# Kernel tuning notes

Measured on AMD Instinct MI355X. Metric: run time of the kernel, lower is better.

Reference implementation:

```python
import jax, jax.numpy as jnp
import numpy as np

B, S, D = 16, 2048, 128


def setup_inputs() -> dict:
    k = jax.random.key(0)
    k1, k2, k3, k4 = jax.random.split(k, 4)
    query = jax.random.normal(k1, (B, S, D), dtype=jnp.float32)
    key = jax.random.normal(k2, (B, S, D), dtype=jnp.float32)
    value = jax.random.normal(k3, (B, S, D), dtype=jnp.float32)
    # per-query tensor-valued inverse scale; shift away from zero for stable division
    inv_scale_factor = jax.random.uniform(k4, (B, S, 1), dtype=jnp.float32) + 0.5
    dropout_p = jnp.float32(0.1)
    return {"query": query, "key": key, "value": value,
            "inv_scale_factor": inv_scale_factor, "dropout_p": dropout_p}


def reference(query, key, value, inv_scale_factor, dropout_p):
    # QK^T: [B, Sq, Sk]
    qk = jnp.einsum('bqd,bkd->bqk', query, key)
    # tensor-valued scale divide (broadcast [B, Sq, 1] over keys)
    scaled_qk = qk / inv_scale_factor
    softmax_qk = jax.nn.softmax(scaled_qk, axis=-1)
    # dropout with a fixed RNG key (deterministic reference)
    keep_prob = 1.0 - dropout_p
    mask = jax.random.bernoulli(jax.random.key(42), keep_prob, softmax_qk.shape)
    dropout_qk = jnp.where(mask, softmax_qk / keep_prob, jnp.float32(0.0))
    # AV: [B, Sq, Dv]
    return jnp.einsum('bqk,bkv->bqv', dropout_qk, value)
```

## Files before the change

kernel.cpp:

```cpp
#include <hip/hip_runtime.h>
#include <stdint.h>


#define B_ 16
#define S_ 2048
#define D_ 128
#define TQ 128
#define TK 64
#define NT (S_ / TK)
#define KSTR 136
#define VSTR 72
#define PSTR 40

typedef float f32x4 __attribute__((ext_vector_type(4)));
typedef _Float16 f16x8 __attribute__((ext_vector_type(8)));
typedef _Float16 f16x2 __attribute__((ext_vector_type(2)));

union F32R { float4 q[4]; float f[16]; };

#define DPP_ROR(x, ctrl) \
  __int_as_float(__builtin_amdgcn_update_dpp(0, __float_as_int(x), (ctrl), 0xf, 0xf, true))
__device__ __forceinline__ float row16_max(float x) {
  x = fmaxf(x, DPP_ROR(x, 0x128));
  x = fmaxf(x, DPP_ROR(x, 0x124));
  x = fmaxf(x, DPP_ROR(x, 0x122));
  x = fmaxf(x, DPP_ROR(x, 0x121));
  return x;
}
__device__ __forceinline__ float row16_sum(float x) {
  x += DPP_ROR(x, 0x128);
  x += DPP_ROR(x, 0x124);
  x += DPP_ROR(x, 0x122);
  x += DPP_ROR(x, 0x121);
  return x;
}

__device__ __forceinline__ uint2 threefry2x32_0_42(uint32_t x0, uint32_t x1) {
  const uint32_t k0 = 0u, k1 = 42u;
  const uint32_t k2 = 0x1BD11BDAu ^ k0 ^ k1;
  x0 += k0; x1 += k1;
#define TFR(r) { x0 += x1; x1 = __builtin_rotateleft32(x1, r); x1 ^= x0; }
  TFR(13) TFR(15) TFR(26) TFR(6)
  x0 += k1; x1 += k2 + 1u;
  TFR(17) TFR(29) TFR(16) TFR(24)
  x0 += k2; x1 += k0 + 2u;
  TFR(13) TFR(15) TFR(26) TFR(6)
  x0 += k0; x1 += k1 + 3u;
  TFR(17) TFR(29) TFR(16) TFR(24)
  x0 += k1; x1 += k2 + 4u;
  TFR(13) TFR(15) TFR(26) TFR(6)
  x0 += k2; x1 += k0 + 5u;
#undef TFR
  return make_uint2(x0, x1);
}

__device__ __forceinline__ uint32_t jax_bits(uint32_t j) {
  const uint2 tf = threefry2x32_0_42(0u, j);
  return tf.x ^ tf.y;
}

__global__ __launch_bounds__(512, 2)
void attn_mfma_kernel(const float* __restrict__ Q, const float* __restrict__ K,
                      const float* __restrict__ V, const float* __restrict__ ISF,
                      const float* __restrict__ DP, float* __restrict__ OUT) {
  extern __shared__ __align__(16) char smem[];
  _Float16* const sK0  = (_Float16*)smem;
  _Float16* const sK1  = (_Float16*)(smem + 17408);
  _Float16* const sVT0 = (_Float16*)(smem + 34816);
  _Float16* const sVT1 = (_Float16*)(smem + 53248);
  _Float16* const sP   = (_Float16*)(smem + 71680);
  float* const sO1 = (float*)smem;
  float* const sM1 = (float*)(smem + 65536);
  float* const sL1 = (float*)(smem + 66048);

  const int t    = threadIdx.x;
  const int lane = t & 63;
  const int l15  = lane & 15;
  const int quad = lane >> 4;
  const int w    = t >> 6;
  const int qg   = w & 3;
  const int kph  = w >> 2;
  const int b    = blockIdx.y;
  const int qb   = blockIdx.x * TQ + qg * 32;

  const float kp = 1.0f - DP[0];
  const uint32_t TH9 = (__float_as_uint(1.0f + kp) & 0x7FFFFFu) << 9;

  float m_[2][4], l_[2][4];
  uint32_t jq[2][4];
  #pragma unroll
  for (int sub = 0; sub < 2; ++sub)
    #pragma unroll
    for (int r = 0; r < 4; ++r) {
      m_[sub][r] = -INFINITY;
      l_[sub][r] = 0.0f;
      jq[sub][r] = ((uint32_t)b << 22)
                 + (uint32_t)(qb + sub * 16 + quad * 4 + r) * (uint32_t)S_;
    }

  f16x8 qf[2][4];
  #pragma unroll
  for (int sub = 0; sub < 2; ++sub) {
    const int qrow = qb + sub * 16 + l15;
    const float qs = 1.4426950408889634f / ISF[b * S_ + qrow];
    const float* qp = Q + ((size_t)(b * S_ + qrow)) * D_;
    #pragma unroll
    for (int c = 0; c < 4; ++c) {
      const float4 a  = *(const float4*)(qp + c * 32 + quad * 8);
      const float4 d2 = *(const float4*)(qp + c * 32 + quad * 8 + 4);
      const float xs[8] = {a.x, a.y, a.z, a.w, d2.x, d2.y, d2.z, d2.w};
      f16x8 h;
      #pragma unroll
      for (int j = 0; j < 8; ++j) h[j] = (_Float16)(xs[j] * qs);
      qf[sub][c] = h;
    }
  }

  f32x4 accO[2][8];
  #pragma unroll
  for (int sub = 0; sub < 2; ++sub)
    #pragma unroll
    for (int i = 0; i < 8; ++i) accO[sub][i] = (f32x4){0.f, 0.f, 0.f, 0.f};

  _Float16* const pwv = &sP[w * 32 * PSTR];

  const int krow = t >> 3, kcol = (t & 7) * 16;
  const int vp = t & 31, dseg = (t >> 5) * 8;

  F32R kreg;
  F32R vreg;

#define ISSUE_LOADS(KT)                                                        \
  {                                                                            \
    const float4* gk4 = (const float4*)(K +                                    \
        ((size_t)(b * S_ + (KT) * TK + krow)) * D_ + kcol);                    \
    _Pragma("unroll") for (int i = 0; i < 4; ++i) kreg.q[i] = gk4[i];          \
    const float4* gv4 = (const float4*)(V +                                    \
        ((size_t)(b * S_ + (KT) * TK + 2 * vp)) * D_ + dseg);                  \
    _Pragma("unroll") for (int i = 0; i < 2; ++i) {                            \
      vreg.q[i] = gv4[i];                                                      \
      vreg.q[i + 2] = gv4[i + 32];             \
    }                                                                          \
  }

#define CONVERT_TO(KB, VB)                                                     \
  {                                                                            \
    _Pragma("unroll") for (int g = 0; g < 2; ++g) {                            \
      f16x8 h;                                                                 \
      _Pragma("unroll") for (int j = 0; j < 8; ++j)                            \
        h[j] = (_Float16)kreg.f[g * 8 + j];                                    \
      *(f16x8*)&(KB)[krow * KSTR + kcol + g * 8] = h;                          \
    }                                                                          \
    _Pragma("unroll") for (int d = 0; d < 8; ++d) {                            \
      f16x2 h = {(_Float16)vreg.f[d], (_Float16)vreg.f[8 + d]};                \
      *(f16x2*)&(VB)[(dseg + d) * VSTR + 2 * vp] = h;                          \
    }                                                                          \
  }

  ISSUE_LOADS(0)
  CONVERT_TO(sK0, sVT0)
  ISSUE_LOADS(1)
  __syncthreads();

  for (int kt = 0; kt < NT; ++kt) {
    const int cur = kt & 1;
    _Float16* const sKc = cur ? sK1 : sK0;
    _Float16* const sVc = cur ? sVT1 : sVT0;

    f32x4 s[2][2];
    #pragma unroll
    for (int n = 0; n < 2; ++n) {
      f32x4 a0 = (f32x4){0.f, 0.f, 0.f, 0.f};
      f32x4 a1 = (f32x4){0.f, 0.f, 0.f, 0.f};
      #pragma unroll
      for (int c = 0; c < 4; ++c) {
        const f16x8 bh = *(const f16x8*)&sKc[(kph * 32 + n * 16 + l15) * KSTR
                                             + c * 32 + quad * 8];
        a0 = __builtin_amdgcn_mfma_f32_16x16x32_f16(qf[0][c], bh, a0, 0, 0, 0);
        a1 = __builtin_amdgcn_mfma_f32_16x16x32_f16(qf[1][c], bh, a1, 0, 0, 0);
      }
      s[0][n] = a0;
      s[1][n] = a1;
    }

    uint32_t rb[2][2][4];
    #pragma unroll
    for (int sub = 0; sub < 2; ++sub)
      #pragma unroll
      for (int n = 0; n < 2; ++n) {
        const uint32_t jcol = (uint32_t)(kt * TK + kph * 32 + n * 16 + l15);
        #pragma unroll
        for (int r = 0; r < 4; ++r)
          rb[sub][n][r] = jax_bits(jq[sub][r] + jcol);
      }

    float mx[2][4];
    int changed = 0;
    #pragma unroll
    for (int sub = 0; sub < 2; ++sub)
      #pragma unroll
      for (int r = 0; r < 4; ++r) {
        mx[sub][r] = row16_max(fmaxf(s[sub][0][r], s[sub][1][r]));
        changed |= (mx[sub][r] > m_[sub][r]);
      }
    if (__ballot(changed) != 0ull) {
      #pragma unroll
      for (int sub = 0; sub < 2; ++sub)
        #pragma unroll
        for (int r = 0; r < 4; ++r) {
          const float mnew = fmaxf(m_[sub][r], mx[sub][r]);
          const float alpha = __builtin_amdgcn_exp2f(m_[sub][r] - mnew);
          m_[sub][r] = mnew;
          l_[sub][r] *= alpha;
          #pragma unroll
          for (int i = 0; i < 8; ++i) accO[sub][i][r] *= alpha;
        }
    }
    #pragma unroll
    for (int sub = 0; sub < 2; ++sub)
      #pragma unroll
      for (int r = 0; r < 4; ++r) {
        const float p0 = __builtin_amdgcn_exp2f(s[sub][0][r] - m_[sub][r]);
        const float p1 = __builtin_amdgcn_exp2f(s[sub][1][r] - m_[sub][r]);
        s[sub][0][r] = p0;
        s[sub][1][r] = p1;
        l_[sub][r] += row16_sum(p0 + p1);
      }

    #pragma unroll
    for (int sub = 0; sub < 2; ++sub)
      #pragma unroll
      for (int n = 0; n < 2; ++n) {
        const int col = n * 16 + l15;
        #pragma unroll
        for (int r = 0; r < 4; ++r) {
          const float pf = (rb[sub][n][r] < TH9) ? s[sub][n][r] : 0.0f;
          pwv[(sub * 16 + quad * 4 + r) * PSTR + col] = (_Float16)pf;
        }
      }
    __threadfence_block();

    {
      const f16x8 ap0 = *(const f16x8*)&pwv[l15 * PSTR + quad * 8];
      const f16x8 ap1 = *(const f16x8*)&pwv[(16 + l15) * PSTR + quad * 8];
      #pragma unroll
      for (int d8 = 0; d8 < 8; ++d8) {
        const f16x8 bv = *(const f16x8*)&sVc[(d8 * 16 + l15) * VSTR
                                             + kph * 32 + quad * 8];
        accO[0][d8] = __builtin_amdgcn_mfma_f32_16x16x32_f16(ap0, bv, accO[0][d8], 0, 0, 0);
        accO[1][d8] = __builtin_amdgcn_mfma_f32_16x16x32_f16(ap1, bv, accO[1][d8], 0, 0, 0);
      }
    }

    if (kt + 1 < NT) {
      _Float16* const sKn = cur ? sK0 : sK1;
      _Float16* const sVn = cur ? sVT0 : sVT1;
      CONVERT_TO(sKn, sVn)
      if (kt + 2 < NT) ISSUE_LOADS(kt + 2)
    }
    __syncthreads();
  }
#undef ISSUE_LOADS
#undef CONVERT_TO

  if (kph == 1) {
    #pragma unroll
    for (int sub = 0; sub < 2; ++sub) {
      if (l15 == 0) {
        #pragma unroll
        for (int r = 0; r < 4; ++r) {
          const int gr = qg * 32 + sub * 16 + quad * 4 + r;
          sM1[gr] = m_[sub][r];
          sL1[gr] = l_[sub][r];
        }
      }
      #pragma unroll
      for (int d8 = 0; d8 < 8; ++d8)
        #pragma unroll
        for (int r = 0; r < 4; ++r) {
          const int gr = qg * 32 + sub * 16 + quad * 4 + r;
          sO1[gr * D_ + d8 * 16 + l15] = accO[sub][d8][r];
        }
    }
  }
  __syncthreads();
  if (kph == 0) {
    #pragma unroll
    for (int sub = 0; sub < 2; ++sub) {
      float a0s[4], a1s[4];
      #pragma unroll
      for (int r = 0; r < 4; ++r) {
        const int gr = qg * 32 + sub * 16 + quad * 4 + r;
        const float m1  = sM1[gr];
        const float l1v = sL1[gr];
        const float mf = fmaxf(m_[sub][r], m1);
        const float a0 = __builtin_amdgcn_exp2f(m_[sub][r] - mf);
        const float a1 = __builtin_amdgcn_exp2f(m1 - mf);
        const float inv = 1.0f / ((a0 * l_[sub][r] + a1 * l1v) * kp);
        a0s[r] = a0 * inv;
        a1s[r] = a1 * inv;
      }
      #pragma unroll
      for (int d8 = 0; d8 < 8; ++d8)
        #pragma unroll
        for (int r = 0; r < 4; ++r) {
          const int gr = qg * 32 + sub * 16 + quad * 4 + r;
          const float o1 = sO1[gr * D_ + d8 * 16 + l15];
          OUT[((size_t)(b * S_ + blockIdx.x * TQ + gr)) * D_ + d8 * 16 + l15] =
              accO[sub][d8][r] * a0s[r] + o1 * a1s[r];
        }
    }
  }
}

extern "C" void kernel_launch(void* const* d_in, const int* in_sizes, int n_in,
                              void* d_out, int out_size, void* d_ws, size_t ws_size,
                              hipStream_t stream) {
  const float* q   = (const float*)d_in[0];
  const float* k   = (const float*)d_in[1];
  const float* v   = (const float*)d_in[2];
  const float* isf = (const float*)d_in[3];
  const float* dp  = (const float*)d_in[4];
  float* out = (float*)d_out;

  dim3 grid(S_ / TQ, B_);
  attn_mfma_kernel<<<grid, dim3(512), 92160, stream>>>(q, k, v, isf, dp, out);
}
```

Before: 276.7 us.

## Use 1024-thread blocks with 4-way key split and 128-key tiles

Doubles the key tile to 128 and the block to 16 waves, so each query group is processed by four key-phase waves instead of two, with a two-level tree merge of partial softmax state through shared memory. V is now single-buffered with an extra barrier per tile, while K stays double-buffered. The aim is to amortize per-tile barriers and raise per-block parallelism. In exchange, LDS per block grows to about 142 KB, which likely leaves one block per CU, and the extra syncs and merge steps add overhead. Dropout indexing depends on the hidden lines and may need adjusting for the new kph range.

After: 627.3 us. 127% more time.

```diff
diff --git a/kernel.cpp b/kernel.cpp
--- a/kernel.cpp
+++ b/kernel.cpp
@@ -6,17 +6,17 @@
 #define S_ 2048
 #define D_ 128
 #define TQ 128
-#define TK 64
+#define TK 128
 #define NT (S_ / TK)
 #define KSTR 136
-#define VSTR 72
+#define VSTR 136
 #define PSTR 40
 
 typedef float f32x4 __attribute__((ext_vector_type(4)));
 typedef _Float16 f16x8 __attribute__((ext_vector_type(8)));
 typedef _Float16 f16x2 __attribute__((ext_vector_type(2)));
 
-union F32R { float4 q[4]; float f[16]; };
+union F32R16 { float4 q[4]; float f[16]; };
 
 #define DPP_ROR(x, ctrl) \
   __int_as_float(__builtin_amdgcn_update_dpp(0, __float_as_int(x), (ctrl), 0xf, 0xf, true))
@@ -59,19 +59,17 @@
   return tf.x ^ tf.y;
 }
 
-__global__ __launch_bounds__(512, 2)
+__global__ __launch_bounds__(1024)
 void attn_mfma_kernel(const float* __restrict__ Q, const float* __restrict__ K,
                       const float* __restrict__ V, const float* __restrict__ ISF,
                       const float* __restrict__ DP, float* __restrict__ OUT) {
   extern __shared__ __align__(16) char smem[];
-  _Float16* const sK0  = (_Float16*)smem;
-  _Float16* const sK1  = (_Float16*)(smem + 17408);
-  _Float16* const sVT0 = (_Float16*)(smem + 34816);
-  _Float16* const sVT1 = (_Float16*)(smem + 53248);
-  _Float16* const sP   = (_Float16*)(smem + 71680);
-  float* const sO1 = (float*)smem;
-  float* const sM1 = (float*)(smem + 65536);
-  float* const sL1 = (float*)(smem + 66048);
+  _Float16* const sK0 = (_Float16*)smem;
+  _Float16* const sK1 = (_Float16*)(smem + 34816);
+  _Float16* const sVT = (_Float16*)(smem + 69632);
+  _Float16* const sP  = (_Float16*)(smem + 104448);
+  float* const sOm  = (float*)smem;
+  float* const sMLm = (float*)(smem + 131072);
 
   const int t    = threadIdx.x;
   const int lane = t & 63;
@@ -125,25 +123,27 @@
   _Float16* const pwv = &sP[w * 32 * PSTR];
 
   const int krow = t >> 3, kcol = (t & 7) * 16;
-  const int vp = t & 31, dseg = (t >> 5) * 8;
-
-  F32R kreg;
-  F32R vreg;
-
-#define ISSUE_LOADS(KT)                                                        \
+  const int vp = t & 63, dseg = (t >> 6) * 8;
+
+  F32R16 kreg;
+  F32R16 vreg;
+
+#define ISSUE_K(KT)                                                            \
   {                                                                            \
     const float4* gk4 = (const float4*)(K +                                    \
         ((size_t)(b * S_ + (KT) * TK + krow)) * D_ + kcol);                    \
     _Pragma("unroll") for (int i = 0; i < 4; ++i) kreg.q[i] = gk4[i];          \
+  }
+#define ISSUE_V(KT)                                                            \
+  {                                                                            \
     const float4* gv4 = (const float4*)(V +                                    \
         ((size_t)(b * S_ + (KT) * TK + 2 * vp)) * D_ + dseg);                  \
-    _Pragma("unroll") for (int i = 0; i < 2; ++i) {                            \
-      vreg.q[i] = gv4[i];                                                      \
-      vreg.q[i + 2] = gv4[i + 32];             \
-    }                                                                          \
-  }
-
-#define CONVERT_TO(KB, VB)                                                     \
+    vreg.q[0] = gv4[0];                                                        \
+    vreg.q[1] = gv4[1];                                                        \
+    vreg.q[2] = gv4[32];                       \
+    vreg.q[3] = gv4[33];                                                       \
+  }
+#define CONV_K(KB)                                                             \
   {                                                                            \
     _Pragma("unroll") for (int g = 0; g < 2; ++g) {                            \
       f16x8 h;                                                                 \
@@ -151,21 +151,32 @@
         h[j] = (_Float16)kreg.f[g * 8 + j];                                    \
       *(f16x8*)&(KB)[krow * KSTR + kcol + g * 8] = h;                          \
     }                                                                          \
+  }
+#define CONV_V()                                                               \
+  {                                                                            \
     _Pragma("unroll") for (int d = 0; d < 8; ++d) {                            \
-      f16x2 h = {(_Float16)vreg.f[d], (_Float16)vreg.f[8 + d]};                \
-      *(f16x2*)&(VB)[(dseg + d) * VSTR + 2 * vp] = h;                          \
+      f16x2 h2 = {(_Float16)vreg.f[d], (_Float16)vreg.f[8 + d]};               \
+      *(f16x2*)&sVT[(dseg + d) * VSTR + 2 * vp] = h2;                          \
     }                                                                          \
   }
 
-  ISSUE_LOADS(0)
-  CONVERT_TO(sK0, sVT0)
-  ISSUE_LOADS(1)
-  __syncthreads();
+  ISSUE_K(0)
+  ISSUE_V(0)
+  CONV_K(sK0)
+  ISSUE_K(1)
 
   for (int kt = 0; kt < NT; ++kt) {
-    const int cur = kt & 1;
-    _Float16* const sKc = cur ? sK1 : sK0;
-    _Float16* const sVc = cur ? sVT1 : sVT0;
+    __syncthreads();
+
+    CONV_V()
+    if (kt + 1 < NT) {
+      _Float16* const sKn = (kt & 1) ? sK0 : sK1;
+      CONV_K(sKn)
+      ISSUE_V(kt + 1)
+      if (kt + 2 < NT) ISSUE_K(kt + 2)
+    }
+
+    _Float16* const sKc = (kt & 1) ? sK1 : sK0;
 
     f32x4 s[2][2];
     #pragma unroll
@@ -239,76 +250,99 @@
         }
       }
     __threadfence_block();
+    __syncthreads();
 
     {
       const f16x8 ap0 = *(const f16x8*)&pwv[l15 * PSTR + quad * 8];
       const f16x8 ap1 = *(const f16x8*)&pwv[(16 + l15) * PSTR + quad * 8];
       #pragma unroll
       for (int d8 = 0; d8 < 8; ++d8) {
-        const f16x8 bv = *(const f16x8*)&sVc[(d8 * 16 + l15) * VSTR
+        const f16x8 bv = *(const f16x8*)&sVT[(d8 * 16 + l15) * VSTR
                                              + kph * 32 + quad * 8];
         accO[0][d8] = __builtin_amdgcn_mfma_f32_16x16x32_f16(ap0, bv, accO[0][d8], 0, 0, 0);
         accO[1][d8] = __builtin_amdgcn_mfma_f32_16x16x32_f16(ap1, bv, accO[1][d8], 0, 0, 0);
       }
     }
-
-    if (kt + 1 < NT) {
-      _Float16* const sKn = cur ? sK0 : sK1;
-      _Float16* const sVn = cur ? sVT0 : sVT1;
-      CONVERT_TO(sKn, sVn)
-      if (kt + 2 < NT) ISSUE_LOADS(kt + 2)
-    }
-    __syncthreads();
-  }
-#undef ISSUE_LOADS
-#undef CONVERT_TO
-
-  if (kph == 1) {
+  }
+#undef ISSUE_K
+#undef ISSUE_V
+#undef CONV_K
+#undef CONV_V
+
+  __syncthreads();
+  if (kph & 1) {
+    const int slot = qg * 2 + (kph >> 1);
+    float* so  = sOm + slot * 4096;
+    float* sml = sMLm + slot * 64;
     #pragma unroll
     for (int sub = 0; sub < 2; ++sub) {
-      if (l15 == 0) {
-        #pragma unroll
-        for (int r = 0; r < 4; ++r) {
-          const int gr = qg * 32 + sub * 16 + quad * 4 + r;
-          sM1[gr] = m_[sub][r];
-          sL1[gr] = l_[sub][r];
-        }
-      }
-      #pragma unroll
-      for (int d8 = 0; d8 < 8; ++d8)
-        #pragma unroll
-        for (int r = 0; r < 4; ++r) {
-          const int gr = qg * 32 + sub * 16 + quad * 4 + r;
-          sO1[gr * D_ + d8 * 16 + l15] = accO[sub][d8][r];
-        }
-    }
+      #pragma unroll
+      for (int r = 0; r < 4; ++r) {
+        const int row = sub * 16 + quad * 4 + r;
+        if (l15 == 0) { sml[row * 2] = m_[sub][r]; sml[row * 2 + 1] = l_[sub][r]; }
+        #pragma unroll
+        for (int d8 = 0; d8 < 8; ++d8)
+          so[row * 128 + d8 * 16 + l15] = accO[sub][d8][r];
+      }
+    }
+  }
+  __syncthreads();
+  if (!(kph & 1)) {
+    const int slot = qg * 2 + (kph >> 1);
+    const float* so  = sOm + slot * 4096;
+    const float* sml = sMLm + slot * 64;
+    #pragma unroll
+    for (int sub = 0; sub < 2; ++sub)
+      #pragma unroll
+      for (int r = 0; r < 4; ++r) {
+        const int row = sub * 16 + quad * 4 + r;
+        const float mp = sml[row * 2], lp = sml[row * 2 + 1];
+        const float mf = fmaxf(m_[sub][r], mp);
+        const float a0 = __builtin_amdgcn_exp2f(m_[sub][r] - mf);
+        const float a1 = __builtin_amdgcn_exp2f(mp - mf);
+        m_[sub][r] = mf;
+        l_[sub][r] = l_[sub][r] * a0 + lp * a1;
+        #pragma unroll
+        for (int d8 = 0; d8 < 8; ++d8)
+          accO[sub][d8][r] = accO[sub][d8][r] * a0 + so[row * 128 + d8 * 16 + l15] * a1;
+      }
+  }
+  __syncthreads();
+  if (kph == 2) {
+    float* so  = sOm + qg * 4096;
+    float* sml = sMLm + qg * 64;
+    #pragma unroll
+    for (int sub = 0; sub < 2; ++sub)
+      #pragma unroll
+      for (int r = 0; r < 4; ++r) {
+        const int row = sub * 16 + quad * 4 + r;
+        if (l15 == 0) { sml[row * 2] = m_[sub][r]; sml[row * 2 + 1] = l_[sub][r]; }
+        #pragma unroll
+        for (int d8 = 0; d8 < 8; ++d8)
+          so[row * 128 + d8 * 16 + l15] = accO[sub][d8][r];
+      }
   }
   __syncthreads();
   if (kph == 0) {
+    const float* so  = sOm + qg * 4096;
+    const float* sml = sMLm + qg * 64;
     #pragma unroll
     for (int sub = 0; sub < 2; ++sub) {
-      float a0s[4], a1s[4];
-      #pragma unroll
-      for (int r = 0; r < 4; ++r) {
-        const int gr = qg * 32 + sub * 16 + quad * 4 + r;
-        const float m1  = sM1[gr];
-        const float l1v = sL1[gr];
-        const float mf = fmaxf(m_[sub][r], m1);
+      #pragma unroll
+      for (int r = 0; r < 4; ++r) {
+        const int row = sub * 16 + quad * 4 + r;
+        const float mp = sml[row * 2], lp = sml[row * 2 + 1];
+        const float mf = fmaxf(m_[sub][r], mp);
         const float a0 = __builtin_amdgcn_exp2f(m_[sub][r] - mf);
-        const float a1 = __builtin_amdgcn_exp2f(m1 - mf);
-        const float inv = 1.0f / ((a0 * l_[sub][r] + a1 * l1v) * kp);
-        a0s[r] = a0 * inv;
-        a1s[r] = a1 * inv;
-      }
-      #pragma unroll
-      for (int d8 = 0; d8 < 8; ++d8)
-        #pragma unroll
-        for (int r = 0; r < 4; ++r) {
-          const int gr = qg * 32 + sub * 16 + quad * 4 + r;
-          const float o1 = sO1[gr * D_ + d8 * 16 + l15];
-          OUT[((size_t)(b * S_ + blockIdx.x * TQ + gr)) * D_ + d8 * 16 + l15] =
-              accO[sub][d8][r] * a0s[r] + o1 * a1s[r];
-        }
+        const float a1 = __builtin_amdgcn_exp2f(mp - mf);
+        const float inv = 1.0f / ((l_[sub][r] * a0 + lp * a1) * kp);
+        const float s0 = a0 * inv, s1 = a1 * inv;
+        const int gr = qg * 32 + row;
+        float* op = OUT + ((size_t)(b * S_ + blockIdx.x * TQ + gr)) * D_;
+        #pragma unroll
+        for (int d8 = 0; d8 < 8; ++d8)
+          op[d8 * 16 + l15] = accO[sub][d8][r] * s0 + so[row * 128 + d8 * 16 + l15] * s1;
+      }
     }
   }
 }
@@ -324,5 +358,5 @@
   float* out = (float*)d_out;
 
   dim3 grid(S_ / TQ, B_);
-  attn_mfma_kernel<<<grid, dim3(512), 92160, stream>>>(q, k, v, isf, dp, out);
-}
+  attn_mfma_kernel<<<grid, dim3(1024), 145408, stream>>>(q, k, v, isf, dp, out);
+}
```

## Halve query tile to 64 rows and single-buffer K/V tiles in LDS

Applied to the files above, without the earlier changes.

Shrinks the query tile from 128 to 64 rows, halves the block to 256 threads and doubles the grid, so each thread loads and converts twice as much K/V per tile. Replaces the double-buffered K and transposed-V LDS tiles with single buffers, guarded by an extra barrier before each conversion, which halves LDS per block. The aim is more blocks per CU and a smaller LDS footprint. The cost is twice the global K/V reads across the grid and a serialized convert step that no longer overlaps with compute.

Result: slower. 307.5 us (+11.1%).

```diff
diff --git a/kernel.cpp b/kernel.cpp
--- a/kernel.cpp
+++ b/kernel.cpp
@@ -5,7 +5,7 @@
 #define B_ 16
 #define S_ 2048
 #define D_ 128
-#define TQ 128
+#define TQ 64
 #define TK 64
 #define NT (S_ / TK)
 #define KSTR 136
@@ -16,7 +16,8 @@
 typedef _Float16 f16x8 __attribute__((ext_vector_type(8)));
 typedef _Float16 f16x2 __attribute__((ext_vector_type(2)));
 
-union F32R { float4 q[4]; float f[16]; };
+union F32R32 { float4 q[8]; float f[32]; };
+union F16R16 { float4 q[4]; float f[16]; };
 
 #define DPP_ROR(x, ctrl) \
   __int_as_float(__builtin_amdgcn_update_dpp(0, __float_as_int(x), (ctrl), 0xf, 0xf, true))
@@ -59,27 +60,25 @@
   return tf.x ^ tf.y;
 }
 
-__global__ __launch_bounds__(512, 2)
+__global__ __launch_bounds__(256, 2)
 void attn_mfma_kernel(const float* __restrict__ Q, const float* __restrict__ K,
                       const float* __restrict__ V, const float* __restrict__ ISF,
                       const float* __restrict__ DP, float* __restrict__ OUT) {
   extern __shared__ __align__(16) char smem[];
-  _Float16* const sK0  = (_Float16*)smem;
-  _Float16* const sK1  = (_Float16*)(smem + 17408);
-  _Float16* const sVT0 = (_Float16*)(smem + 34816);
-  _Float16* const sVT1 = (_Float16*)(smem + 53248);
-  _Float16* const sP   = (_Float16*)(smem + 71680);
+  _Float16* const sK  = (_Float16*)smem;
+  _Float16* const sVT = (_Float16*)(smem + 17408);
+  _Float16* const sP  = (_Float16*)(smem + 35840);
   float* const sO1 = (float*)smem;
-  float* const sM1 = (float*)(smem + 65536);
-  float* const sL1 = (float*)(smem + 66048);
+  float* const sM1 = (float*)(smem + 32768);
+  float* const sL1 = (float*)(smem + 33024);
 
   const int t    = threadIdx.x;
   const int lane = t & 63;
   const int l15  = lane & 15;
   const int quad = lane >> 4;
   const int w    = t >> 6;
-  const int qg   = w & 3;
-  const int kph  = w >> 2;
+  const int qg   = w & 1;
+  const int kph  = w >> 1;
   const int b    = blockIdx.y;
   const int qb   = blockIdx.x * TQ + qg * 32;
 
@@ -124,49 +123,45 @@
 
   _Float16* const pwv = &sP[w * 32 * PSTR];
 
-  const int krow = t >> 3, kcol = (t & 7) * 16;
-  const int vp = t & 31, dseg = (t >> 5) * 8;
-
-  F32R kreg;
-  F32R vreg;
+  const int krow = t >> 2, kcol = (t & 3) * 32;
+  const int vp = t & 31, dseg = (t >> 5) * 16;
+
+  F32R32 kreg;
+  F16R16 vreg0, vreg1;
 
 #define ISSUE_LOADS(KT)                                                        \
   {                                                                            \
     const float4* gk4 = (const float4*)(K +                                    \
         ((size_t)(b * S_ + (KT) * TK + krow)) * D_ + kcol);                    \
-    _Pragma("unroll") for (int i = 0; i < 4; ++i) kreg.q[i] = gk4[i];          \
+    _Pragma("unroll") for (int i = 0; i < 8; ++i) kreg.q[i] = gk4[i];          \
     const float4* gv4 = (const float4*)(V +                                    \
         ((size_t)(b * S_ + (KT) * TK + 2 * vp)) * D_ + dseg);                  \
-    _Pragma("unroll") for (int i = 0; i < 2; ++i) {                            \
-      vreg.q[i] = gv4[i];                                                      \
-      vreg.q[i + 2] = gv4[i + 32];             \
+    _Pragma("unroll") for (int i = 0; i < 4; ++i) {                            \
+      vreg0.q[i] = gv4[i];                                                     \
+      vreg1.q[i] = gv4[i + 32];                \
     }                                                                          \
   }
 
-#define CONVERT_TO(KB, VB)                                                     \
+#define CONVERT_TILES()                                                        \
   {                                                                            \
-    _Pragma("unroll") for (int g = 0; g < 2; ++g) {                            \
+    _Pragma("unroll") for (int g = 0; g < 4; ++g) {                            \
       f16x8 h;                                                                 \
       _Pragma("unroll") for (int j = 0; j < 8; ++j)                            \
         h[j] = (_Float16)kreg.f[g * 8 + j];                                    \
-      *(f16x8*)&(KB)[krow * KSTR + kcol + g * 8] = h;                          \
+      *(f16x8*)&sK[krow * KSTR + kcol + g * 8] = h;                            \
     }                                                                          \
-    _Pragma("unroll") for (int d = 0; d < 8; ++d) {                            \
-      f16x2 h = {(_Float16)vreg.f[d], (_Float16)vreg.f[8 + d]};                \
-      *(f16x2*)&(VB)[(dseg + d) * VSTR + 2 * vp] = h;                          \
+    _Pragma("unroll") for (int d = 0; d < 16; ++d) {                           \
+      f16x2 h2 = {(_Float16)vreg0.f[d], (_Float16)vreg1.f[d]};                 \
+      *(f16x2*)&sVT[(dseg + d) * VSTR + 2 * vp] = h2;                          \
     }                                                                          \
   }
 
   ISSUE_LOADS(0)
-  CONVERT_TO(sK0, sVT0)
+  CONVERT_TILES()
   ISSUE_LOADS(1)
   __syncthreads();
 
   for (int kt = 0; kt < NT; ++kt) {
-    const int cur = kt & 1;
-    _Float16* const sKc = cur ? sK1 : sK0;
-    _Float16* const sVc = cur ? sVT1 : sVT0;
-
     f32x4 s[2][2];
     #pragma unroll
     for (int n = 0; n < 2; ++n) {
@@ -174,8 +169,8 @@
       f32x4 a1 = (f32x4){0.f, 0.f, 0.f, 0.f};
       #pragma unroll
       for (int c = 0; c < 4; ++c) {
-        const f16x8 bh = *(const f16x8*)&sKc[(kph * 32 + n * 16 + l15) * KSTR
-                                             + c * 32 + quad * 8];
+        const f16x8 bh = *(const f16x8*)&sK[(kph * 32 + n * 16 + l15) * KSTR
+                                            + c * 32 + quad * 8];
         a0 = __builtin_amdgcn_mfma_f32_16x16x32_f16(qf[0][c], bh, a0, 0, 0, 0);
         a1 = __builtin_amdgcn_mfma_f32_16x16x32_f16(qf[1][c], bh, a1, 0, 0, 0);
       }
@@ -245,7 +240,7 @@
       const f16x8 ap1 = *(const f16x8*)&pwv[(16 + l15) * PSTR + quad * 8];
       #pragma unroll
       for (int d8 = 0; d8 < 8; ++d8) {
-        const f16x8 bv = *(const f16x8*)&sVc[(d8 * 16 + l15) * VSTR
+        const f16x8 bv = *(const f16x8*)&sVT[(d8 * 16 + l15) * VSTR
                                              + kph * 32 + quad * 8];
         accO[0][d8] = __builtin_amdgcn_mfma_f32_16x16x32_f16(ap0, bv, accO[0][d8], 0, 0, 0);
         accO[1][d8] = __builtin_amdgcn_mfma_f32_16x16x32_f16(ap1, bv, accO[1][d8], 0, 0, 0);
@@ -253,16 +248,16 @@
     }
 
     if (kt + 1 < NT) {
-      _Float16* const sKn = cur ? sK0 : sK1;
-      _Float16* const sVn = cur ? sVT0 : sVT1;
-      CONVERT_TO(sKn, sVn)
+      __syncthreads();
+      CONVERT_TILES()
       if (kt + 2 < NT) ISSUE_LOADS(kt + 2)
-    }
-    __syncthreads();
+      __syncthreads();
+    }
   }
 #undef ISSUE_LOADS
-#undef CONVERT_TO
-
+#undef CONVERT_TILES
+
+  __syncthreads();
   if (kph == 1) {
     #pragma unroll
     for (int sub = 0; sub < 2; ++sub) {
@@ -324,5 +319,5 @@
   float* out = (float*)d_out;
 
   dim3 grid(S_ / TQ, B_);
-  attn_mfma_kernel<<<grid, dim3(512), 92160, stream>>>(q, k, v, isf, dp, out);
-}
+  attn_mfma_kernel<<<grid, dim3(256), 46080, stream>>>(q, k, v, isf, dp, out);
+}
```
